# Performance work log

Hardware: AMD Instinct MI355X
Metric: run time of the kernel (lower is better)

Reference implementation:

```python
import jax, jax.numpy as jnp
import numpy as np

HEADDIM = 128
CHUNK = 256


def _ssd_scan(x, dt, A, B, C, chunk):
    # x: (b,l,h,p)  dt: (b,l,h)  A: (h,)  B,C: (b,l,n)  (single group g=1 shared by all heads)
    b, l, h, p = x.shape
    n = B.shape[-1]
    nc = l // chunk
    dA = dt * A  # (b,l,h)
    xc = x.reshape(b, nc, chunk, h, p)
    dtc = dt.reshape(b, nc, chunk, h)
    dAc = dA.reshape(b, nc, chunk, h)
    Bc = B.reshape(b, nc, chunk, n)
    Cc = C.reshape(b, nc, chunk, n)
    cs = jnp.cumsum(dAc, axis=2)  # (b,nc,c,h) cumulative log-decay within chunk
    # intra-chunk quadratic part
    CB = jnp.einsum('bjin,bjkn->bjik', Cc, Bc)  # (b,nc,c,c)
    decay = jnp.exp(cs[:, :, :, None, :] - cs[:, :, None, :, :])  # (b,nc,i,k,h)
    mask = jnp.tril(jnp.ones((chunk, chunk), dtype=bool))
    decay = jnp.where(mask[None, None, :, :, None], decay, 0.0)
    y_intra = jnp.einsum('bjik,bjikh,bjkh,bjkhp->bjihp', CB, decay, dtc, xc)
    # per-chunk end states
    decay_states = jnp.exp(cs[:, :, -1:, :] - cs)  # (b,nc,c,h)
    states = jnp.einsum('bjkh,bjkh,bjkn,bjkhp->bjhnp', decay_states, dtc, Bc, xc)
    # recurrence across chunks: h_j = exp(sum dA_j) * h_{j-1} + states_j
    chunk_decay = jnp.exp(cs[:, :, -1, :])  # (b,nc,h)
    def step(carry, inp):
        s, d = inp
        new = carry * d[:, :, None, None] + s
        return new, carry  # emit state BEFORE this chunk
    init = jnp.zeros((b, h, n, p), x.dtype)
    _, prev = jax.lax.scan(step, init,
                           (states.transpose(1, 0, 2, 3, 4), chunk_decay.transpose(1, 0, 2)))
    prev = prev.transpose(1, 0, 2, 3, 4)  # (b,nc,h,n,p)
    y_inter = jnp.einsum('bjih,bjin,bjhnp->bjihp', jnp.exp(cs), Cc, prev)
    return (y_intra + y_inter).reshape(b, l, h, p)


def setup_inputs() -> dict:
    key = jax.random.key(0)
    k1, k2, k3, k4 = jax.random.split(key, 4)
    b, l, d_inner, nheads, d_state = 2, 4096, 2048, 16, 256
    x = jax.random.normal(k1, (b, l, d_inner), dtype=jnp.float32)
    BC = jax.random.normal(k2, (b, l, 2 * d_state), dtype=jnp.float32) * 0.1
    dt = jax.random.normal(k3, (b, l, 2 * nheads), dtype=jnp.float32) - 3.0
    A_log = jnp.zeros((nheads,), dtype=jnp.float32)
    D = jnp.ones((nheads,), dtype=jnp.float32)
    W_fcD = jax.random.normal(k4, (nheads, d_inner), dtype=jnp.float32) * 0.02
    return {"x": x, "BC": BC, "dt": dt, "A_log": A_log, "D": D, "W_fcD": W_fcD}


def reference(x, BC, dt, A_log, D, W_fcD):
    b, l, dim = x.shape
    h = A_log.shape[0]
    p = HEADDIM
    d_state = BC.shape[-1] // 2
    A = -jnp.exp(A_log)
    # bidirectional: concat forward stream with time-flipped backward stream along batch
    dt2 = jnp.concatenate((dt[:, :, :h], jnp.flip(dt[:, :, h:], axis=1)), axis=0)
    dt2 = jax.nn.softplus(dt2)
    x_og = x
    x2 = jnp.concatenate((x, jnp.flip(x, axis=1)), axis=0)
    BC2 = jnp.concatenate((BC, jnp.flip(BC, axis=1)), axis=0)
    B, C = BC2[..., :d_state], BC2[..., d_state:]
    y = _ssd_scan(x2.reshape(2 * b, l, h, p), dt2, A, B, C, CHUNK)
    y = y.reshape(2 * b, l, dim)
    y = jnp.roll(y, shift=1, axis=1).at[:, 0, :].set(0.0)
    y_fw, y_bw = y[:b], jnp.flip(y[b:], axis=1)
    gate = x_og @ W_fcD.T + D  # (b,l,h)
    y = y_fw + y_bw + x_og * jnp.repeat(gate, p, axis=-1)
    return y
```

## Files before the change

### kernel.cpp

```cpp
#include <hip/hip_runtime.h>
#include <stdint.h>

#define NB 2
#define SL 4096
#define NH 16
#define HD 128
#define DS 256
#define CK 256
#define NCH 16
#define NSQ 4
#define DI 2048

typedef unsigned short u16;
typedef unsigned int u32;
typedef __attribute__((ext_vector_type(8))) __bf16 bf16x8;
typedef __attribute__((ext_vector_type(4))) float f32x4;

__device__ __forceinline__ int tor(int dir, int t) { return dir ? (SL - 1 - t) : t; }

__device__ __forceinline__ u16 f2bf(float f) {
  u32 u = __float_as_uint(f);
  u = u + 0x7fffu + ((u >> 16) & 1u);
  return (u16)(u >> 16);
}
__device__ __forceinline__ float bf2f(u16 s) {
  return __uint_as_float(((u32)s) << 16);
}

__device__ __forceinline__ void gl_lds16(const u16* g, u16* l) {
  __builtin_amdgcn_global_load_lds((const __attribute__((address_space(1))) u32*)g,
                                   (__attribute__((address_space(3))) u32*)l, 16, 0, 0);
}

__device__ __forceinline__ void stage_tile(const u16* __restrict__ src, u16* lds,
                                           int lane, int w, int k0) {
  int sgrow = lane >> 2, sc = lane & 3;
  int r0 = w << 5;
  int ra = r0 + sgrow, rb = ra + 16;
  int kqa = (sc ^ ((ra >> 1) & 3)) << 3;
  int kqb = (sc ^ ((rb >> 1) & 3)) << 3;
  gl_lds16(src + (size_t)ra * 256 + k0 + kqa, lds + r0 * 32);
  gl_lds16(src + (size_t)rb * 256 + k0 + kqb, lds + (r0 + 16) * 32);
}

__device__ __forceinline__ bf16x8 frag(const u16* lds, int base_row, int m, int quad) {
  int row = base_row + m;
  return *(const bf16x8*)&lds[row * 32 + ((quad ^ ((row >> 1) & 3)) << 3)];
}

__device__ __forceinline__ void mfma16(const u16* As, const u16* Bs, int wi, int wp,
                                       int m, int quad, f32x4 acc[4][4]) {
  bf16x8 af[4], bv[4];
#pragma unroll
  for (int r = 0; r < 4; ++r) af[r] = frag(As, wi + (r << 4), m, quad);
#pragma unroll
  for (int c = 0; c < 4; ++c) bv[c] = frag(Bs, wp + (c << 4), m, quad);
#pragma unroll
  for (int r = 0; r < 4; ++r)
#pragma unroll
    for (int c = 0; c < 4; ++c)
      acc[r][c] = __builtin_amdgcn_mfma_f32_16x16x32_bf16(af[r], bv[c], acc[r][c], 0, 0, 0);
}

__global__ __launch_bounds__(256) void kprep(const float* __restrict__ dt,
                                             const float* __restrict__ A_log,
                                             float* __restrict__ csb,
                                             float* __restrict__ dtvb,
                                             float* __restrict__ cdecb) {
  int blk = blockIdx.x;
  int h = blk & 15, sj = blk >> 4;
  int s = sj >> 4, j = sj & 15;
  int b = s & 1, dir = s >> 1;
  int i = threadIdx.x;
  int to = tor(dir, j * CK + i);
  __shared__ float sbuf[CK];
  float a = -expf(A_log[h]);
  float raw = dt[((size_t)(b * SL + to)) * (2 * NH) + dir * NH + h];
  float sp = (raw > 20.f) ? raw : log1pf(expf(raw));
  sbuf[i] = sp * a;
  __syncthreads();
  for (int off = 1; off < CK; off <<= 1) {
    float v = (i >= off) ? sbuf[i - off] : 0.f;
    __syncthreads();
    sbuf[i] += v;
    __syncthreads();
  }
  float csv = sbuf[i];
  size_t base = ((size_t)sj * NH + h) * CK;
  csb[base + i] = csv;
  dtvb[base + i] = sp;
  if (i == CK - 1) cdecb[sj * NH + h] = expf(csv);
}

__global__ __launch_bounds__(256) void kcast(const float* __restrict__ BC,
                                             u16* __restrict__ Bbf,
                                             u16* __restrict__ Cbf) {
  int blk = blockIdx.x;
  int s = blk >> 12, t = blk & (SL - 1);
  int b = s & 1, dir = s >> 1;
  int tsrc = tor(dir, t);
  int tid = threadIdx.x;
  const float* src = BC + ((size_t)(b * SL + tsrc)) * (2 * DS);
  size_t dstb = ((size_t)s * SL + t) * DS;
  Bbf[dstb + tid] = f2bf(src[tid]);
  Cbf[dstb + tid] = f2bf(src[DS + tid]);
}

__global__ __launch_bounds__(256) void ktransB(const u16* __restrict__ Bbf,
                                               u16* __restrict__ BbfT) {
  int sj = blockIdx.x;
  int s = sj >> 4, j = sj & 15;
  __shared__ u16 T[64 * 264];
  int tid = threadIdx.x;
  const u16* src = Bbf + ((size_t)s * SL + j * CK) * DS;
  u16* dst = BbfT + (size_t)sj * DS * CK;
  int kr = tid >> 2, part = (tid & 3) * 64;
  for (int k0 = 0; k0 < CK; k0 += 64) {
    __syncthreads();
    {
      const uint4* gs = (const uint4*)(src + (size_t)(k0 + kr) * DS + part);
      uint4* tb = (uint4*)&T[kr * 264 + part];
#pragma unroll
      for (int q = 0; q < 8; ++q) tb[q] = gs[q];
    }
    __syncthreads();
    int n = tid;
    u16 col[64];
#pragma unroll
    for (int kq = 0; kq < 64; ++kq) col[kq] = T[kq * 264 + n];
    uint4* ds_ = (uint4*)(dst + (size_t)n * CK + k0);
#pragma unroll
    for (int q = 0; q < 8; ++q) {
      uint4 wv;
      wv.x = (u32)col[q * 8 + 0] | ((u32)col[q * 8 + 1] << 16);
      wv.y = (u32)col[q * 8 + 2] | ((u32)col[q * 8 + 3] << 16);
      wv.z = (u32)col[q * 8 + 4] | ((u32)col[q * 8 + 5] << 16);
      wv.w = (u32)col[q * 8 + 6] | ((u32)col[q * 8 + 7] << 16);
      ds_[q] = wv;
    }
  }
}

__global__ __launch_bounds__(256) void kxsT(const float* __restrict__ xg,
                                            const float* __restrict__ csb,
                                            const float* __restrict__ dtvb,
                                            u16* __restrict__ xsT) {
  int inst = blockIdx.x;
  int h = inst & 15, sj = inst >> 4;
  int s = sj >> 4, j = sj & 15;
  int b = s & 1, dir = s >> 1;
  int tid = threadIdx.x;
  __shared__ u16 Ls[128 * 40];
  size_t cbase = ((size_t)sj * NH + h) * CK;
  u16* dst = xsT + (size_t)inst * (128 * 256);
  int kk = tid >> 3;
  int pg = (tid & 7) * 16;
  int p2 = tid >> 1, half = tid & 1;
  for (int k0 = 0; k0 < CK; k0 += 32) {
    int kglob = k0 + kk;
    float sc_ = expf(-csb[cbase + kglob]) * dtvb[cbase + kglob];
    int t = tor(dir, j * CK + kglob);
    const float* src = xg + ((size_t)(b * SL + t)) * DI + h * HD + pg;
    float4 v0 = ((const float4*)src)[0];
    float4 v1 = ((const float4*)src)[1];
    float4 v2 = ((const float4*)src)[2];
    float4 v3 = ((const float4*)src)[3];
    float vv[16] = {v0.x, v0.y, v0.z, v0.w, v1.x, v1.y, v1.z, v1.w,
                    v2.x, v2.y, v2.z, v2.w, v3.x, v3.y, v3.z, v3.w};
    __syncthreads();
#pragma unroll
    for (int q = 0; q < 16; ++q) Ls[(pg + q) * 40 + kk] = f2bf(vv[q] * sc_);
    __syncthreads();
    uint4 w0 = *(const uint4*)&Ls[p2 * 40 + half * 16];
    uint4 w1 = *(const uint4*)&Ls[p2 * 40 + half * 16 + 8];
    *(uint4*)&dst[(size_t)p2 * 256 + k0 + half * 16] = w0;
    *(uint4*)&dst[(size_t)p2 * 256 + k0 + half * 16 + 8] = w1;
  }
}

__global__ __launch_bounds__(256) void kcb(const u16* __restrict__ Cbf,
                                           const u16* __restrict__ Bbf,
                                           u16* __restrict__ CBm) {
  int blk = blockIdx.x;
  int tri = blk % 3;
  int sj = blk / 3;
  int it0 = tri ? 128 : 0;
  int kt0 = (tri == 2) ? 128 : 0;
  int s = sj >> 4, j = sj & 15;
  __shared__ u16 As[128 * 32];
  __shared__ u16 Bs[128 * 32];
  int tid = threadIdx.x;
  int w = tid >> 6, lane = tid & 63;
  int wi = (w >> 1) << 6, wp = (w & 1) << 6;
  int m = lane & 15, quad = lane >> 4;
  const u16* Ab = Cbf + ((size_t)s * SL + j * CK + it0) * DS;
  const u16* Bb = Bbf + ((size_t)s * SL + j * CK + kt0) * DS;
  f32x4 zini = {0.f, 0.f, 0.f, 0.f};
  f32x4 acc[4][4];
#pragma unroll
  for (int r = 0; r < 4; ++r)
#pragma unroll
    for (int c = 0; c < 4; ++c) acc[r][c] = zini;
  for (int ks = 0; ks < 8; ++ks) {
    int k0 = ks << 5;
    stage_tile(Ab, As, lane, w, k0);
    stage_tile(Bb, Bs, lane, w, k0);
    __syncthreads();
    mfma16(As, Bs, wi, wp, m, quad, acc);
    __syncthreads();
  }
  int diag = (it0 == kt0);
  u16* dst = CBm + ((size_t)sj * CK + it0) * CK + kt0;
#pragma unroll
  for (int r = 0; r < 4; ++r)
#pragma unroll
    for (int rg = 0; rg < 4; ++rg) {
      int irow = wi + (r << 4) + (quad << 2) + rg;
#pragma unroll
      for (int c = 0; c < 4; ++c) {
        int kcol = wp + (c << 4) + m;
        float v = acc[r][c][rg];
        if (diag && kcol > irow) v = 0.f;
        dst[(size_t)irow * CK + kcol] = f2bf(v);
      }
    }
}

__global__ __launch_bounds__(256) void kstates(const u16* __restrict__ xsT,
                                               const u16* __restrict__ BbfT,
                                               const float* __restrict__ cdecb,
                                               u16* __restrict__ prevT) {
  int blk = blockIdx.x;
  int ntile = blk & 1;
  int inst = blk >> 1;
  int h = inst & 15, sj = inst >> 4;
  int nt0 = ntile << 7;
  __shared__ u16 As[128 * 32];
  __shared__ u16 Bs[128 * 32];
  int tid = threadIdx.x;
  int w = tid >> 6, lane = tid & 63;
  int wi = (w >> 1) << 6, wp = (w & 1) << 6;
  int m = lane & 15, quad = lane >> 4;
  const u16* Ab = xsT + (size_t)inst * (128 * 256);
  const u16* Bb = BbfT + ((size_t)sj * DS + nt0) * CK;
  f32x4 zini = {0.f, 0.f, 0.f, 0.f};
  f32x4 acc[4][4];
#pragma unroll
  for (int r = 0; r < 4; ++r)
#pragma unroll
    for (int c = 0; c < 4; ++c) acc[r][c] = zini;
  for (int ks = 0; ks < 8; ++ks) {
    int k0 = ks << 5;
    stage_tile(Ab, As, lane, w, k0);
    stage_tile(Bb, Bs, lane, w, k0);
    __syncthreads();
    mfma16(As, Bs, wi, wp, m, quad, acc);
    __syncthreads();
  }
  float scale = cdecb[sj * NH + h];
  u16* dst = prevT + (size_t)inst * (128 * 256) + nt0;
#pragma unroll
  for (int r = 0; r < 4; ++r)
#pragma unroll
    for (int rg = 0; rg < 4; ++rg) {
      int prow = wi + (r << 4) + (quad << 2) + rg;
#pragma unroll
      for (int c = 0; c < 4; ++c) {
        int ncol = wp + (c << 4) + m;
        dst[(size_t)prow * 256 + ncol] = f2bf(acc[r][c][rg] * scale);
      }
    }
}

__global__ __launch_bounds__(256) void kscan(u16* __restrict__ prevT,
                                             const float* __restrict__ cdecb) {
  int g = blockIdx.x * 256 + threadIdx.x;
  int n = g & 255;
  int p = (g >> 8) & 127;
  int h = (g >> 15) & 15;
  int s = g >> 19;
  size_t base = (((size_t)(s * 256 + h) * 128) + p) * 256 + n;
  const size_t stride = (size_t)NH * 128 * 256;
  float carry = 0.f;
  for (int j = 0; j < NCH; ++j) {
    size_t idx = base + (size_t)j * stride;
    float sv = bf2f(prevT[idx]);
    prevT[idx] = f2bf(carry);
    carry = carry * cdecb[(s * NCH + j) * NH + h] + sv;
  }
}

__global__ __launch_bounds__(256) void ky(const u16* __restrict__ CBm,
                                          const u16* __restrict__ Cbf,
                                          const u16* __restrict__ xsT,
                                          const u16* __restrict__ prevT,
                                          const float* __restrict__ csb,
                                          u16* __restrict__ ytmpb) {
  int blk = blockIdx.x;
  int itile = blk & 1;
  int inst = blk >> 1;
  int h = inst & 15, sj = inst >> 4;
  int s = sj >> 4, j = sj & 15;
  int it0 = itile << 7;
  __shared__ u16 As[128 * 32];
  __shared__ u16 Bs[128 * 32];
  int tid = threadIdx.x;
  int w = tid >> 6, lane = tid & 63;
  int wi = (w >> 1) << 6, wp = (w & 1) << 6;
  int m = lane & 15, quad = lane >> 4;

  const u16* Ai = CBm + ((size_t)sj * CK + it0) * CK;
  const u16* Ae = Cbf + ((size_t)s * SL + j * CK + it0) * DS;
  const u16* Bi = xsT + (size_t)inst * (128 * 256);
  const u16* Be = prevT + (size_t)inst * (128 * 256);

  int nIntra = itile ? 8 : 4;
  int nTot = nIntra + 8;

  f32x4 zini = {0.f, 0.f, 0.f, 0.f};
  f32x4 acc[4][4];
#pragma unroll
  for (int r = 0; r < 4; ++r)
#pragma unroll
    for (int c = 0; c < 4; ++c) acc[r][c] = zini;

  for (int ks = 0; ks < nTot; ++ks) {
    int intra = ks < nIntra;
    int k0 = (intra ? ks : ks - nIntra) << 5;
    const u16* Ab = intra ? Ai : Ae;
    const u16* Bb = intra ? Bi : Be;
    stage_tile(Ab, As, lane, w, k0);
    stage_tile(Bb, Bs, lane, w, k0);
    __syncthreads();
    mfma16(As, Bs, wi, wp, m, quad, acc);
    __syncthreads();
  }
  const float* csrow = csb + ((size_t)sj * NH + h) * CK + it0;
  u16* yb = ytmpb + ((size_t)s * SL + j * CK + it0) * DI + h * HD;
#pragma unroll
  for (int r = 0; r < 4; ++r)
#pragma unroll
    for (int rg = 0; rg < 4; ++rg) {
      int irow = wi + (r << 4) + (quad << 2) + rg;
      float esc = expf(csrow[irow]);
#pragma unroll
      for (int c = 0; c < 4; ++c) {
        int pcol = wp + (c << 4) + m;
        yb[(size_t)irow * DI + pcol] = f2bf(acc[r][c][rg] * esc);
      }
    }
}

__device__ __forceinline__ void unpk8(uint4 u, float* o) {
  o[0] = __uint_as_float(u.x << 16); o[1] = __uint_as_float(u.x & 0xffff0000u);
  o[2] = __uint_as_float(u.y << 16); o[3] = __uint_as_float(u.y & 0xffff0000u);
  o[4] = __uint_as_float(u.z << 16); o[5] = __uint_as_float(u.z & 0xffff0000u);
  o[6] = __uint_as_float(u.w << 16); o[7] = __uint_as_float(u.w & 0xffff0000u);
}

__global__ __launch_bounds__(256) void kfinal(const float* __restrict__ xg,
                                              const float* __restrict__ Wg,
                                              const float* __restrict__ Dg,
                                              const u16* __restrict__ ytmpb,
                                              float* __restrict__ out) {
  int bid = blockIdx.x;
  int b = bid >> 12;
  int t = bid & (SL - 1);
  __shared__ float xrow[DI];
  __shared__ float gp[4][NH];
  __shared__ float gate[NH];
  int tid = threadIdx.x;
  const float* xr = xg + ((size_t)(b * SL + t)) * DI;
  ((float4*)xrow)[tid] = ((const float4*)xr)[tid];
  ((float4*)xrow)[tid + 256] = ((const float4*)xr)[tid + 256];
  __syncthreads();
  float a[NH];
#pragma unroll
  for (int h = 0; h < NH; ++h) a[h] = 0.f;
#pragma unroll
  for (int q = 0; q < 8; ++q) {
    int d = q * 256 + tid;
    float xv = xrow[d];
#pragma unroll
    for (int h = 0; h < NH; ++h) a[h] += xv * Wg[h * DI + d];
  }
#pragma unroll
  for (int h = 0; h < NH; ++h) {
    float v = a[h];
    v += __shfl_down(v, 32);
    v += __shfl_down(v, 16);
    v += __shfl_down(v, 8);
    v += __shfl_down(v, 4);
    v += __shfl_down(v, 2);
    v += __shfl_down(v, 1);
    if ((tid & 63) == 0) gp[tid >> 6][h] = v;
  }
  __syncthreads();
  if (tid < NH) gate[tid] = gp[0][tid] + gp[1][tid] + gp[2][tid] + gp[3][tid] + Dg[tid];
  __syncthreads();
  int d0 = tid * 8;
  float g = gate[tid >> 4];
  float fy[8] = {0.f, 0.f, 0.f, 0.f, 0.f, 0.f, 0.f, 0.f};
  float by[8] = {0.f, 0.f, 0.f, 0.f, 0.f, 0.f, 0.f, 0.f};
  if (t > 0) {
    uint4 u = *(const uint4*)(ytmpb + ((size_t)(b * SL + (t - 1))) * DI + d0);
    unpk8(u, fy);
  }
  if (t < SL - 1) {
    uint4 u = *(const uint4*)(ytmpb + ((size_t)((2 + b) * SL + (SL - 2 - t))) * DI + d0);
    unpk8(u, by);
  }
  float* op = out + ((size_t)(b * SL + t)) * DI + d0;
#pragma unroll
  for (int q = 0; q < 8; ++q)
    op[q] = fy[q] + by[q] + xrow[d0 + q] * g;
}

extern "C" void kernel_launch(void* const* d_in, const int* in_sizes, int n_in,
                              void* d_out, int out_size, void* d_ws, size_t ws_size,
                              hipStream_t stream) {
  (void)in_sizes; (void)n_in; (void)out_size; (void)ws_size;
  const float* x     = (const float*)d_in[0];
  const float* BC    = (const float*)d_in[1];
  const float* dt    = (const float*)d_in[2];
  const float* A_log = (const float*)d_in[3];
  const float* Dg    = (const float*)d_in[4];
  const float* W     = (const float*)d_in[5];
  float* out = (float*)d_out;

  char* p = (char*)d_ws;
  float* cs   = (float*)p;  p += (size_t)NSQ * NCH * NH * CK * 4;
  float* dtv  = (float*)p;  p += (size_t)NSQ * NCH * NH * CK * 4;
  float* cdec = (float*)p;  p += (size_t)NSQ * NCH * NH * 4;
  u16* Bbf    = (u16*)p;    p += (size_t)NSQ * SL * DS * 2;
  u16* Cbf    = (u16*)p;    p += (size_t)NSQ * SL * DS * 2;
  u16* BbfT   = (u16*)p;    p += (size_t)NSQ * NCH * DS * CK * 2;
  u16* CBm    = (u16*)p;    p += (size_t)NSQ * NCH * CK * CK * 2;
  u16* xsT    = (u16*)p;    p += (size_t)NSQ * NCH * NH * HD * CK * 2;
  u16* prevT  = (u16*)p;    p += (size_t)NSQ * NCH * NH * HD * DS * 2;
  u16* ytmpb  = (u16*)p;    p += (size_t)NSQ * SL * DI * 2;

  hipLaunchKernelGGL(kprep,   dim3(NSQ * NCH * NH),      dim3(CK),  0, stream, dt, A_log, cs, dtv, cdec);
  hipLaunchKernelGGL(kcast,   dim3(NSQ * SL),            dim3(256), 0, stream, BC, Bbf, Cbf);
  hipLaunchKernelGGL(ktransB, dim3(NSQ * NCH),           dim3(256), 0, stream, Bbf, BbfT);
  hipLaunchKernelGGL(kxsT,    dim3(NSQ * NCH * NH),      dim3(256), 0, stream, x, cs, dtv, xsT);
  hipLaunchKernelGGL(kcb,     dim3(NSQ * NCH * 3),       dim3(256), 0, stream, Cbf, Bbf, CBm);
  hipLaunchKernelGGL(kstates, dim3(NSQ * NCH * NH * 2),  dim3(256), 0, stream, xsT, BbfT, cdec, prevT);
  hipLaunchKernelGGL(kscan,   dim3(NSQ * NH * HD * DS / 256), dim3(256), 0, stream, prevT, cdec);
  hipLaunchKernelGGL(ky,      dim3(NSQ * NCH * NH * 2),  dim3(256), 0, stream, CBm, Cbf, xsT, prevT, cs, ytmpb);
  hipLaunchKernelGGL(kfinal,  dim3(NB * SL),             dim3(256), 0, stream, x, W, Dg, ytmpb, out);
}
```

Baseline: 415.1 us.

## Stage GEMM epilogues through LDS, vectorize scan, split gate projection into separate kernel

The kcb, kstates and ky epilogues now write bf16 results into a padded shared-memory tile and then copy them to global memory as 16-byte rows, replacing scattered 2-byte stores. kscan has each thread handle 8 contiguous state elements with vectorized loads and stores. The gate projection moves out of the per-row final kernel into a transposed-weight kgate kernel that processes 8 rows per wave, and the final combine uses float4 loads and stores. This adds two launches and a gate buffer in the workspace.

After: 420.1 us. Within noise of the previous version (+1.2%).

```diff
diff --git a/kernel.cpp b/kernel.cpp
--- a/kernel.cpp
+++ b/kernel.cpp
@@ -10,6 +10,8 @@
 #define NCH 16
 #define NSQ 4
 #define DI 2048
+
+#define EPST 132
 
 typedef unsigned short u16;
 typedef unsigned int u32;
@@ -187,8 +189,9 @@
   int it0 = tri ? 128 : 0;
   int kt0 = (tri == 2) ? 128 : 0;
   int s = sj >> 4, j = sj & 15;
-  __shared__ u16 As[128 * 32];
-  __shared__ u16 Bs[128 * 32];
+  __shared__ u16 smem[128 * EPST];
+  u16* As = smem;
+  u16* Bs = smem + 4096;
   int tid = threadIdx.x;
   int w = tid >> 6, lane = tid & 63;
   int wi = (w >> 1) << 6, wp = (w & 1) << 6;
@@ -210,7 +213,6 @@
     __syncthreads();
   }
   int diag = (it0 == kt0);
-  u16* dst = CBm + ((size_t)sj * CK + it0) * CK + kt0;
 #pragma unroll
   for (int r = 0; r < 4; ++r)
 #pragma unroll
@@ -221,9 +223,18 @@
         int kcol = wp + (c << 4) + m;
         float v = acc[r][c][rg];
         if (diag && kcol > irow) v = 0.f;
-        dst[(size_t)irow * CK + kcol] = f2bf(v);
+        smem[irow * EPST + kcol] = f2bf(v);
       }
     }
+  __syncthreads();
+  {
+    u16* dstb = CBm + ((size_t)sj * CK + it0) * CK + kt0;
+    int rr = tid >> 1, off = (tid & 1) << 6;
+    const uint4* srcv = (const uint4*)&smem[rr * EPST + off];
+    uint4* dstv = (uint4*)(dstb + (size_t)rr * CK + off);
+#pragma unroll
+    for (int q = 0; q < 8; ++q) dstv[q] = srcv[q];
+  }
 }
 
 __global__ __launch_bounds__(256) void kstates(const u16* __restrict__ xsT,
@@ -235,8 +246,9 @@
   int inst = blk >> 1;
   int h = inst & 15, sj = inst >> 4;
   int nt0 = ntile << 7;
-  __shared__ u16 As[128 * 32];
-  __shared__ u16 Bs[128 * 32];
+  __shared__ u16 smem[128 * EPST];
+  u16* As = smem;
+  u16* Bs = smem + 4096;
   int tid = threadIdx.x;
   int w = tid >> 6, lane = tid & 63;
   int wi = (w >> 1) << 6, wp = (w & 1) << 6;
@@ -258,7 +270,6 @@
     __syncthreads();
   }
   float scale = cdecb[sj * NH + h];
-  u16* dst = prevT + (size_t)inst * (128 * 256) + nt0;
 #pragma unroll
   for (int r = 0; r < 4; ++r)
 #pragma unroll
@@ -267,26 +278,49 @@
 #pragma unroll
       for (int c = 0; c < 4; ++c) {
         int ncol = wp + (c << 4) + m;
-        dst[(size_t)prow * 256 + ncol] = f2bf(acc[r][c][rg] * scale);
+        smem[prow * EPST + ncol] = f2bf(acc[r][c][rg] * scale);
       }
     }
+  __syncthreads();
+  {
+    u16* dstb = prevT + (size_t)inst * (128 * 256) + nt0;
+    int rr = tid >> 1, off = (tid & 1) << 6;
+    const uint4* srcv = (const uint4*)&smem[rr * EPST + off];
+    uint4* dstv = (uint4*)(dstb + (size_t)rr * 256 + off);
+#pragma unroll
+    for (int q = 0; q < 8; ++q) dstv[q] = srcv[q];
+  }
 }
 
 __global__ __launch_bounds__(256) void kscan(u16* __restrict__ prevT,
                                              const float* __restrict__ cdecb) {
   int g = blockIdx.x * 256 + threadIdx.x;
-  int n = g & 255;
-  int p = (g >> 8) & 127;
-  int h = (g >> 15) & 15;
-  int s = g >> 19;
-  size_t base = (((size_t)(s * 256 + h) * 128) + p) * 256 + n;
+  int n0 = (g & 31) * 8;
+  int p = (g >> 5) & 127;
+  int h = (g >> 12) & 15;
+  int s = g >> 16;
+  size_t base = ((size_t)(s * 256 + h) * 128 + p) * 256 + n0;
   const size_t stride = (size_t)NH * 128 * 256;
-  float carry = 0.f;
+  float carry[8] = {0.f, 0.f, 0.f, 0.f, 0.f, 0.f, 0.f, 0.f};
   for (int j = 0; j < NCH; ++j) {
     size_t idx = base + (size_t)j * stride;
-    float sv = bf2f(prevT[idx]);
-    prevT[idx] = f2bf(carry);
-    carry = carry * cdecb[(s * NCH + j) * NH + h] + sv;
+    uint4 u = *(const uint4*)&prevT[idx];
+    u32 uu[4] = {u.x, u.y, u.z, u.w};
+    float sv[8];
+#pragma unroll
+    for (int q = 0; q < 4; ++q) {
+      sv[2 * q] = __uint_as_float(uu[q] << 16);
+      sv[2 * q + 1] = __uint_as_float(uu[q] & 0xffff0000u);
+    }
+    uint4 wv;
+    wv.x = (u32)f2bf(carry[0]) | ((u32)f2bf(carry[1]) << 16);
+    wv.y = (u32)f2bf(carry[2]) | ((u32)f2bf(carry[3]) << 16);
+    wv.z = (u32)f2bf(carry[4]) | ((u32)f2bf(carry[5]) << 16);
+    wv.w = (u32)f2bf(carry[6]) | ((u32)f2bf(carry[7]) << 16);
+    *(uint4*)&prevT[idx] = wv;
+    float d = cdecb[(s * NCH + j) * NH + h];
+#pragma unroll
+    for (int q = 0; q < 8; ++q) carry[q] = carry[q] * d + sv[q];
   }
 }
 
@@ -302,8 +336,9 @@
   int h = inst & 15, sj = inst >> 4;
   int s = sj >> 4, j = sj & 15;
   int it0 = itile << 7;
-  __shared__ u16 As[128 * 32];
-  __shared__ u16 Bs[128 * 32];
+  __shared__ u16 smem[128 * EPST];
+  u16* As = smem;
+  u16* Bs = smem + 4096;
   int tid = threadIdx.x;
   int w = tid >> 6, lane = tid & 63;
   int wi = (w >> 1) << 6, wp = (w & 1) << 6;
@@ -336,7 +371,6 @@
     __syncthreads();
   }
   const float* csrow = csb + ((size_t)sj * NH + h) * CK + it0;
-  u16* yb = ytmpb + ((size_t)s * SL + j * CK + it0) * DI + h * HD;
 #pragma unroll
   for (int r = 0; r < 4; ++r)
 #pragma unroll
@@ -346,9 +380,59 @@
 #pragma unroll
       for (int c = 0; c < 4; ++c) {
         int pcol = wp + (c << 4) + m;
-        yb[(size_t)irow * DI + pcol] = f2bf(acc[r][c][rg] * esc);
+        smem[irow * EPST + pcol] = f2bf(acc[r][c][rg] * esc);
       }
     }
+  __syncthreads();
+  {
+    u16* yb = ytmpb + ((size_t)s * SL + j * CK + it0) * DI + h * HD;
+    int rr = tid >> 1, off = (tid & 1) << 6;
+    const uint4* srcv = (const uint4*)&smem[rr * EPST + off];
+    uint4* dstv = (uint4*)(yb + (size_t)rr * DI + off);
+#pragma unroll
+    for (int q = 0; q < 8; ++q) dstv[q] = srcv[q];
+  }
+}
+
+__global__ __launch_bounds__(256) void kwt(const float* __restrict__ Wg,
+                                           float* __restrict__ WT) {
+  int g = blockIdx.x * 256 + threadIdx.x;
+  int d = g >> 4, h = g & 15;
+  WT[g] = Wg[(size_t)h * DI + d];
+}
+
+__global__ __launch_bounds__(256) void kgate(const float* __restrict__ xg,
+                                             const float* __restrict__ WT,
+                                             const float* __restrict__ Dg,
+                                             float* __restrict__ gate) {
+  int wave = (blockIdx.x * 256 + threadIdx.x) >> 6;
+  int lane = threadIdx.x & 63;
+  int gg = lane >> 4, h = lane & 15;
+  int row0 = wave * 8;
+  const float* xb = xg + (size_t)row0 * DI;
+  float acc[8] = {0.f, 0.f, 0.f, 0.f, 0.f, 0.f, 0.f, 0.f};
+  for (int q = 0; q < 128; ++q) {
+    int d = gg * 4 + 16 * q;
+    float w0 = WT[(d + 0) * 16 + h];
+    float w1 = WT[(d + 1) * 16 + h];
+    float w2 = WT[(d + 2) * 16 + h];
+    float w3 = WT[(d + 3) * 16 + h];
+#pragma unroll
+    for (int r = 0; r < 8; ++r) {
+      float4 xv = *(const float4*)&xb[(size_t)r * DI + d];
+      acc[r] += xv.x * w0 + xv.y * w1 + xv.z * w2 + xv.w * w3;
+    }
+  }
+#pragma unroll
+  for (int r = 0; r < 8; ++r) {
+    acc[r] += __shfl_down(acc[r], 32);
+    acc[r] += __shfl_down(acc[r], 16);
+  }
+  if (lane < 16) {
+    float dv = Dg[h];
+#pragma unroll
+    for (int r = 0; r < 8; ++r) gate[(size_t)(row0 + r) * NH + h] = acc[r] + dv;
+  }
 }
 
 __device__ __forceinline__ void unpk8(uint4 u, float* o) {
@@ -358,48 +442,16 @@
   o[6] = __uint_as_float(u.w << 16); o[7] = __uint_as_float(u.w & 0xffff0000u);
 }
 
-__global__ __launch_bounds__(256) void kfinal(const float* __restrict__ xg,
-                                              const float* __restrict__ Wg,
-                                              const float* __restrict__ Dg,
-                                              const u16* __restrict__ ytmpb,
-                                              float* __restrict__ out) {
+__global__ __launch_bounds__(256) void kcombine(const float* __restrict__ xg,
+                                                const float* __restrict__ gate,
+                                                const u16* __restrict__ ytmpb,
+                                                float* __restrict__ out) {
   int bid = blockIdx.x;
   int b = bid >> 12;
   int t = bid & (SL - 1);
-  __shared__ float xrow[DI];
-  __shared__ float gp[4][NH];
-  __shared__ float gate[NH];
-  int tid = threadIdx.x;
-  const float* xr = xg + ((size_t)(b * SL + t)) * DI;
-  ((float4*)xrow)[tid] = ((const float4*)xr)[tid];
-  ((float4*)xrow)[tid + 256] = ((const float4*)xr)[tid + 256];
-  __syncthreads();
-  float a[NH];
-#pragma unroll
-  for (int h = 0; h < NH; ++h) a[h] = 0.f;
-#pragma unroll
-  for (int q = 0; q < 8; ++q) {
-    int d = q * 256 + tid;
-    float xv = xrow[d];
-#pragma unroll
-    for (int h = 0; h < NH; ++h) a[h] += xv * Wg[h * DI + d];
-  }
-#pragma unroll
-  for (int h = 0; h < NH; ++h) {
-    float v = a[h];
-    v += __shfl_down(v, 32);
-    v += __shfl_down(v, 16);
-    v += __shfl_down(v, 8);
-    v += __shfl_down(v, 4);
-    v += __shfl_down(v, 2);
-    v += __shfl_down(v, 1);
-    if ((tid & 63) == 0) gp[tid >> 6][h] = v;
-  }
-  __syncthreads();
-  if (tid < NH) gate[tid] = gp[0][tid] + gp[1][tid] + gp[2][tid] + gp[3][tid] + Dg[tid];
-  __syncthreads();
+  int tid = threadIdx.x;
   int d0 = tid * 8;
-  float g = gate[tid >> 4];
+  float g = gate[(size_t)(b * SL + t) * NH + (tid >> 4)];
   float fy[8] = {0.f, 0.f, 0.f, 0.f, 0.f, 0.f, 0.f, 0.f};
   float by[8] = {0.f, 0.f, 0.f, 0.f, 0.f, 0.f, 0.f, 0.f};
   if (t > 0) {
@@ -410,10 +462,18 @@
     uint4 u = *(const uint4*)(ytmpb + ((size_t)((2 + b) * SL + (SL - 2 - t))) * DI + d0);
     unpk8(u, by);
   }
+  const float* xr = xg + ((size_t)(b * SL + t)) * DI + d0;
+  float4 x0 = ((const float4*)xr)[0];
+  float4 x1 = ((const float4*)xr)[1];
+  float xa[8] = {x0.x, x0.y, x0.z, x0.w, x1.x, x1.y, x1.z, x1.w};
   float* op = out + ((size_t)(b * SL + t)) * DI + d0;
-#pragma unroll
-  for (int q = 0; q < 8; ++q)
-    op[q] = fy[q] + by[q] + xrow[d0 + q] * g;
+  float4 o0, o1;
+  o0.x = fy[0] + by[0] + xa[0] * g; o0.y = fy[1] + by[1] + xa[1] * g;
+  o0.z = fy[2] + by[2] + xa[2] * g; o0.w = fy[3] + by[3] + xa[3] * g;
+  o1.x = fy[4] + by[4] + xa[4] * g; o1.y = fy[5] + by[5] + xa[5] * g;
+  o1.z = fy[6] + by[6] + xa[6] * g; o1.w = fy[7] + by[7] + xa[7] * g;
+  ((float4*)op)[0] = o0;
+  ((float4*)op)[1] = o1;
 }
 
 extern "C" void kernel_launch(void* const* d_in, const int* in_sizes, int n_in,
@@ -432,6 +492,8 @@
   float* cs   = (float*)p;  p += (size_t)NSQ * NCH * NH * CK * 4;
   float* dtv  = (float*)p;  p += (size_t)NSQ * NCH * NH * CK * 4;
   float* cdec = (float*)p;  p += (size_t)NSQ * NCH * NH * 4;
+  float* WT   = (float*)p;  p += (size_t)DI * NH * 4;
+  float* gateb= (float*)p;  p += (size_t)NB * SL * NH * 4;
   u16* Bbf    = (u16*)p;    p += (size_t)NSQ * SL * DS * 2;
   u16* Cbf    = (u16*)p;    p += (size_t)NSQ * SL * DS * 2;
   u16* BbfT   = (u16*)p;    p += (size_t)NSQ * NCH * DS * CK * 2;
@@ -445,8 +507,10 @@
   hipLaunchKernelGGL(ktransB, dim3(NSQ * NCH),           dim3(256), 0, stream, Bbf, BbfT);
   hipLaunchKernelGGL(kxsT,    dim3(NSQ * NCH * NH),      dim3(256), 0, stream, x, cs, dtv, xsT);
   hipLaunchKernelGGL(kcb,     dim3(NSQ * NCH * 3),       dim3(256), 0, stream, Cbf, Bbf, CBm);
+  hipLaunchKernelGGL(kwt,     dim3(DI * NH / 256),       dim3(256), 0, stream, W, WT);
+  hipLaunchKernelGGL(kgate,   dim3(NB * SL / 32),        dim3(256), 0, stream, x, WT, Dg, gateb);
   hipLaunchKernelGGL(kstates, dim3(NSQ * NCH * NH * 2),  dim3(256), 0, stream, xsT, BbfT, cdec, prevT);
-  hipLaunchKernelGGL(kscan,   dim3(NSQ * NH * HD * DS / 256), dim3(256), 0, stream, prevT, cdec);
+  hipLaunchKernelGGL(kscan,   dim3(NSQ * NH * HD * DS / (256 * 8)), dim3(256), 0, stream, prevT, cdec);
   hipLaunchKernelGGL(ky,      dim3(NSQ * NCH * NH * 2),  dim3(256), 0, stream, CBm, Cbf, xsT, prevT, cs, ytmpb);
-  hipLaunchKernelGGL(kfinal,  dim3(NB * SL),             dim3(256), 0, stream, x, W, Dg, ytmpb, out);
-}
+  hipLaunchKernelGGL(kcombine,dim3(NB * SL),             dim3(256), 0, stream, x, gateb, ytmpb, out);
+}
```
